# Kernel tuning notes

Hardware: AMD Instinct MI355X
Metric: run time of the kernel (lower is better)

Reference implementation:

```python
import jax, jax.numpy as jnp
import numpy as np

DROPOUT_P = 0.5


def normalize_adj(A):
    # A_tilda = A + I ; A_hat = D^-0.5 A_tilda D^-0.5
    # The torch code does this with diag_embed + two bmm (O(N^3));
    # mathematically it is row/col broadcasting (O(N^2)).
    B, N, _ = A.shape
    A_tilda = A + jnp.eye(N, dtype=A.dtype)
    d_inv_sqrt = jnp.sum(A_tilda, axis=2) ** -0.5          # [B, N]
    return d_inv_sqrt[:, :, None] * A_tilda * d_inv_sqrt[:, None, :]


def gcn_layer(X, A_hat, W, b):
    # standard Kipf GCN layer: A_hat @ (X @ W) + b
    return jnp.einsum('bnm,bmd->bnd', A_hat, X @ W) + b


def setup_inputs() -> dict:
    key = jax.random.key(0)
    ks = jax.random.split(key, 6)
    B, N, Din, H, C = 8, 2048, 64, 64, 16
    X = jax.random.normal(ks[0], (B, N, Din), dtype=jnp.float32)
    A = jax.random.uniform(ks[1], (B, N, N), dtype=jnp.float32)
    W1 = jax.random.normal(ks[2], (Din, H), dtype=jnp.float32) * (1.0 / np.sqrt(Din))
    b1 = jax.random.normal(ks[3], (H,), dtype=jnp.float32) * 0.01
    W2 = jax.random.normal(ks[4], (H, C), dtype=jnp.float32) * (1.0 / np.sqrt(H))
    b2 = jax.random.normal(ks[5], (C,), dtype=jnp.float32) * 0.01
    return {"X": X, "A": A, "W1": W1, "b1": b1, "W2": W2, "b2": b2}


def reference(X, A, W1, b1, W2, b2):
    A_hat = normalize_adj(A)
    h = jax.nn.relu(gcn_layer(X, A_hat, W1, b1))
    # F.dropout default training=True -> apply dropout with a fixed key
    keep = jax.random.bernoulli(jax.random.key(42), 1.0 - DROPOUT_P, h.shape)
    h = jnp.where(keep, h / (1.0 - DROPOUT_P), 0.0).astype(h.dtype)
    return gcn_layer(h, A_hat, W2, b2)
```

## Files before the change

kernel.cpp:

```cpp
#include <hip/hip_runtime.h>

#define BN 16384
#define NN 2048
#define DD 64
#define CC 16
#define KS1 8
#define KS2 16

typedef short bf16x8 __attribute__((ext_vector_type(8)));
typedef float f32x4 __attribute__((ext_vector_type(4)));
typedef unsigned short u16x4 __attribute__((ext_vector_type(4)));

__device__ __forceinline__ f32x4 mfma16(bf16x8 a, bf16x8 b, f32x4 c) {
  return __builtin_amdgcn_mfma_f32_16x16x32_bf16(a, b, c, 0, 0, 0);
}
__device__ __forceinline__ unsigned short f2bf(float f) {
  unsigned u = __float_as_uint(f);
  return (unsigned short)((u + 0x7FFFu + ((u >> 16) & 1u)) >> 16);
}
__device__ __forceinline__ float bf2f(unsigned short h) {
  return __uint_as_float(((unsigned)h) << 16);
}

__device__ __forceinline__ unsigned tf_bits(unsigned i) {
  unsigned x0 = 0u;
  unsigned x1 = i;
  const unsigned k0 = 0u, k1 = 42u, k2 = 0x1BD11BDAu ^ 0u ^ 42u;
  x0 += k0; x1 += k1;
#define TFR(r) { x0 += x1; x1 = (x1 << (r)) | (x1 >> (32 - (r))); x1 ^= x0; }
  TFR(13) TFR(15) TFR(26) TFR(6)
  x0 += k1; x1 += k2 + 1u;
  TFR(17) TFR(29) TFR(16) TFR(24)
  x0 += k2; x1 += k0 + 2u;
  TFR(13) TFR(15) TFR(26) TFR(6)
  x0 += k0; x1 += k1 + 3u;
  TFR(17) TFR(29) TFR(16) TFR(24)
  x0 += k1; x1 += k2 + 4u;
  TFR(13) TFR(15) TFR(26) TFR(6)
  x0 += k2; x1 += k0 + 5u;
#undef TFR
  return x0 ^ x1;
}


__global__ __launch_bounds__(256) void k_deg(const float* __restrict__ A,
    float* __restrict__ dis, unsigned short* __restrict__ Abf)
{
  const int w = threadIdx.x >> 6, lane = threadIdx.x & 63;
  const size_t row = (size_t)blockIdx.x * 4 + w;
  const float4* Arow = (const float4*)(A + row * NN);
  unsigned short* Brow = Abf + row * NN;
  float s = 0.f;
#pragma unroll
  for (int it = 0; it < 8; ++it) {
    float4 v = Arow[lane + 64 * it];
    s += (v.x + v.y) + (v.z + v.w);
    u16x4 p = { f2bf(v.x), f2bf(v.y), f2bf(v.z), f2bf(v.w) };
    *(u16x4*)(Brow + lane * 4 + it * 256) = p;
  }
#pragma unroll
  for (int m = 32; m; m >>= 1) s += __shfl_xor(s, m, 64);
  if (lane == 0) dis[row] = 1.0f / sqrtf(s + 1.0f);
}

__global__ __launch_bounds__(256) void k_xw1(const float* __restrict__ X,
    const float* __restrict__ W1, const float* __restrict__ dis,
    unsigned short* __restrict__ Y1s, unsigned short* __restrict__ Y1sT)
{
  const int tid = threadIdx.x;
  const int w = __builtin_amdgcn_readfirstlane(tid >> 6);
  const int lane = tid & 63;
  const int m15 = lane & 15, quad = lane >> 4;
  const int r0 = blockIdx.x * 64;
  const int b = r0 >> 11, kr0 = r0 & (NN - 1);
  const int arow = r0 + w * 16 + m15;
  const f32x4 zero = 0.f;
  f32x4 acc[4];
#pragma unroll
  for (int t = 0; t < 4; ++t) acc[t] = zero;
#pragma unroll
  for (int ksx = 0; ksx < 2; ++ksx) {
    const float* xp = X + (size_t)arow * DD + ksx * 32 + quad * 8;
    float4 x0 = *(const float4*)xp;
    float4 x1 = *(const float4*)(xp + 4);
    bf16x8 af = { (short)f2bf(x0.x), (short)f2bf(x0.y), (short)f2bf(x0.z), (short)f2bf(x0.w),
                  (short)f2bf(x1.x), (short)f2bf(x1.y), (short)f2bf(x1.z), (short)f2bf(x1.w) };
#pragma unroll
    for (int t = 0; t < 4; ++t) {
      const float* wp = W1 + (size_t)(ksx * 32 + quad * 8) * DD + t * 16 + m15;
      bf16x8 bfr = { (short)f2bf(wp[0*DD]), (short)f2bf(wp[1*DD]), (short)f2bf(wp[2*DD]), (short)f2bf(wp[3*DD]),
                     (short)f2bf(wp[4*DD]), (short)f2bf(wp[5*DD]), (short)f2bf(wp[6*DD]), (short)f2bf(wp[7*DD]) };
      acc[t] = mfma16(af, bfr, acc[t]);
    }
  }
#pragma unroll
  for (int t = 0; t < 4; ++t)
#pragma unroll
    for (int r = 0; r < 4; ++r) {
      const int rowo = r0 + w * 16 + quad * 4 + r;
      const unsigned short v = f2bf(dis[rowo] * acc[t][r]);
      Y1s[(size_t)rowo * DD + t * 16 + m15] = v;
      Y1sT[((size_t)b * DD + t * 16 + m15) * NN + (kr0 + w * 16 + quad * 4 + r)] = v;
    }
}

__global__ __launch_bounds__(256, 4) void k_gemm1(const unsigned short* __restrict__ Abf,
    const unsigned short* __restrict__ Y1sT, float* __restrict__ Z1)
{
  const int Mb = blockIdx.x >> 4;
  const int ns = (blockIdx.x >> 3) & 1;
  const int ks = blockIdx.x & 7;
  const int w = __builtin_amdgcn_readfirstlane((int)threadIdx.x >> 6);
  const int lane = threadIdx.x & 63;
  const int m15 = lane & 15, quad = lane >> 4;
  const int b = Mb >> 3;
  const int k0 = ks * 256 + quad * 8;
  const unsigned short* Ap[4];
#pragma unroll
  for (int m = 0; m < 4; ++m)
    Ap[m] = Abf + ((size_t)Mb * 256 + m * 64 + w * 16 + m15) * NN + k0;
  const unsigned short* Bp0 = Y1sT + ((size_t)b * DD + ns * 32 + m15) * NN + k0;
  const unsigned short* Bp1 = Bp0 + (size_t)16 * NN;
  const f32x4 zero = 0.f;
  f32x4 acc[4][2];
#pragma unroll
  for (int m = 0; m < 4; ++m) { acc[m][0] = zero; acc[m][1] = zero; }
  bf16x8 a[4], b0, b1;
#pragma unroll
  for (int m = 0; m < 4; ++m) a[m] = *(const bf16x8*)Ap[m];
  b0 = *(const bf16x8*)Bp0;
  b1 = *(const bf16x8*)Bp1;
#pragma unroll 1
  for (int kk = 0; kk < 8; ++kk) {
    const int off = (kk < 7) ? (kk + 1) * 32 : 0;
    bf16x8 na[4], nb0, nb1;
#pragma unroll
    for (int m = 0; m < 4; ++m) na[m] = *(const bf16x8*)(Ap[m] + off);
    nb0 = *(const bf16x8*)(Bp0 + off);
    nb1 = *(const bf16x8*)(Bp1 + off);
#pragma unroll
    for (int m = 0; m < 4; ++m) {
      acc[m][0] = mfma16(a[m], b0, acc[m][0]);
      acc[m][1] = mfma16(a[m], b1, acc[m][1]);
    }
#pragma unroll
    for (int m = 0; m < 4; ++m) a[m] = na[m];
    b0 = nb0; b1 = nb1;
  }
#pragma unroll
  for (int m = 0; m < 4; ++m)
#pragma unroll
    for (int t = 0; t < 2; ++t)
#pragma unroll
      for (int r = 0; r < 4; ++r)
        Z1[((size_t)ks * BN + Mb * 256 + m * 64 + w * 16 + quad * 4 + r) * DD
           + ns * 32 + t * 16 + m15] = acc[m][t][r];
}

__global__ __launch_bounds__(256) void k_epi1(const float* __restrict__ Z1,
    const unsigned short* __restrict__ Y1s, const float* __restrict__ dis,
    const float* __restrict__ b1, const float* __restrict__ W2,
    unsigned short* __restrict__ Y2sT)
{
  __shared__ float hs[64 * 65];
  __shared__ float W2l[DD * CC];
  const int tid = threadIdx.x;
  const int r0 = blockIdx.x * 64;
  const int b = r0 >> 11, kr0 = r0 & (NN - 1);
  *(float4*)(W2l + tid * 4) = *(const float4*)(W2 + tid * 4);
  const int n = tid & 63, wg = tid >> 6;
  const float bias = b1[n];
#pragma unroll
  for (int i = 0; i < 16; ++i) {
    const int rl = wg * 16 + i;
    const size_t row = (size_t)r0 + rl;
    const size_t o = row * DD + n;
    float z = bf2f(Y1s[o]);
#pragma unroll
    for (int p = 0; p < KS1; ++p) z += Z1[((size_t)p * BN + row) * DD + n];
    float h = fmaxf(dis[row] * z + bias, 0.f);
    const unsigned bits = tf_bits((unsigned)o);
    h = (bits >> 31) ? 0.f : (h + h);
    hs[rl * 65 + n] = h;
  }
  __syncthreads();
  const int c = tid & 15, rg = tid >> 4;
  float y[4];
#pragma unroll
  for (int rr = 0; rr < 4; ++rr) {
    const int rl = rg * 4 + rr;
    float s = 0.f;
#pragma unroll
    for (int k = 0; k < 64; ++k) s += hs[rl * 65 + k] * W2l[k * CC + c];
    y[rr] = dis[r0 + rl] * s;
  }
  u16x4 pk = { f2bf(y[0]), f2bf(y[1]), f2bf(y[2]), f2bf(y[3]) };
  *(u16x4*)(Y2sT + ((size_t)b * CC + c) * NN + kr0 + rg * 4) = pk;
}

__global__ __launch_bounds__(256, 4) void k_gemm2(const unsigned short* __restrict__ Abf,
    const unsigned short* __restrict__ Y2sT, float* __restrict__ Z2)
{
  const int Mb = blockIdx.x >> 4;
  const int ks = blockIdx.x & 15;
  const int w = __builtin_amdgcn_readfirstlane((int)threadIdx.x >> 6);
  const int lane = threadIdx.x & 63;
  const int m15 = lane & 15, quad = lane >> 4;
  const int b = Mb >> 3;
  const int k0 = ks * 128 + quad * 8;
  const unsigned short* Ap[4];
#pragma unroll
  for (int m = 0; m < 4; ++m)
    Ap[m] = Abf + ((size_t)Mb * 256 + m * 64 + w * 16 + m15) * NN + k0;
  const unsigned short* Bp = Y2sT + ((size_t)b * CC + m15) * NN + k0;
  const f32x4 zero = 0.f;
  f32x4 acc[4];
#pragma unroll
  for (int m = 0; m < 4; ++m) acc[m] = zero;
  bf16x8 a[4], bb;
#pragma unroll
  for (int m = 0; m < 4; ++m) a[m] = *(const bf16x8*)Ap[m];
  bb = *(const bf16x8*)Bp;
#pragma unroll 1
  for (int kk = 0; kk < 4; ++kk) {
    const int off = (kk < 3) ? (kk + 1) * 32 : 0;
    bf16x8 na[4], nbb;
#pragma unroll
    for (int m = 0; m < 4; ++m) na[m] = *(const bf16x8*)(Ap[m] + off);
    nbb = *(const bf16x8*)(Bp + off);
#pragma unroll
    for (int m = 0; m < 4; ++m) acc[m] = mfma16(a[m], bb, acc[m]);
#pragma unroll
    for (int m = 0; m < 4; ++m) a[m] = na[m];
    bb = nbb;
  }
#pragma unroll
  for (int m = 0; m < 4; ++m)
#pragma unroll
    for (int r = 0; r < 4; ++r)
      Z2[((size_t)ks * BN + Mb * 256 + m * 64 + w * 16 + quad * 4 + r) * CC + m15] = acc[m][r];
}

__global__ __launch_bounds__(256) void k_final(const float* __restrict__ Z2,
    const unsigned short* __restrict__ Y2sT, const float* __restrict__ dis,
    const float* __restrict__ b2, float* __restrict__ out)
{
  const int r = blockIdx.x * 256 + threadIdx.x;
  const int b = r >> 11, kr = r & (NN - 1);
  float s[16];
#pragma unroll
  for (int c = 0; c < 16; ++c) s[c] = bf2f(Y2sT[((size_t)b * CC + c) * NN + kr]);
#pragma unroll
  for (int p = 0; p < KS2; ++p)
#pragma unroll
    for (int q = 0; q < 4; ++q) {
      float4 v = *(const float4*)(Z2 + ((size_t)p * BN + r) * CC + q * 4);
      s[q*4+0] += v.x; s[q*4+1] += v.y; s[q*4+2] += v.z; s[q*4+3] += v.w;
    }
  const float dv = dis[r];
#pragma unroll
  for (int q = 0; q < 4; ++q) {
    float4 o4;
    o4.x = dv * s[q*4+0] + b2[q*4+0];
    o4.y = dv * s[q*4+1] + b2[q*4+1];
    o4.z = dv * s[q*4+2] + b2[q*4+2];
    o4.w = dv * s[q*4+3] + b2[q*4+3];
    *(float4*)(out + (size_t)r * CC + q * 4) = o4;
  }
}

#define FKS1 4
#define FKS2 16

__global__ __launch_bounds__(256) void d_deg_xw(const float* __restrict__ A,
    const float* __restrict__ X, const float* __restrict__ W1,
    float* __restrict__ dis, float* __restrict__ Y1s)
{
  const int w = threadIdx.x >> 6, lane = threadIdx.x & 63;
  const int row = __builtin_amdgcn_readfirstlane(blockIdx.x * 4 + w);
  const float4* Arow = (const float4*)(A + (size_t)row * NN);
  float s = 0.f;
#pragma unroll
  for (int it = 0; it < 8; ++it) {
    float4 v = Arow[lane + 64 * it];
    s += v.x + v.y + v.z + v.w;
  }
#pragma unroll
  for (int m = 32; m; m >>= 1) s += __shfl_xor(s, m, 64);
  const float dv = 1.0f / sqrtf(s + 1.0f);
  if (lane == 0) dis[row] = dv;
  const float* Xr = X + (size_t)row * DD;
  float acc = 0.f;
#pragma unroll
  for (int k = 0; k < DD; ++k) acc += Xr[k] * W1[k * DD + lane];
  Y1s[(size_t)row * DD + lane] = dv * acc;
}

__global__ __launch_bounds__(256) void d_gemm1(const float* __restrict__ A,
    const float* __restrict__ Y1s, float* __restrict__ Z1)
{
  const int rb = blockIdx.x >> 2, ks = blockIdx.x & (FKS1 - 1);
  const int lane = threadIdx.x & 63;
  const int c0 = __builtin_amdgcn_readfirstlane((threadIdx.x >> 6) << 4);
  const int row = rb * 64 + lane;
  const int batch = rb >> 5;
  const int KSEG = NN / FKS1;
  const float* Arow = A + (size_t)row * NN + ks * KSEG;
  const float* Yb = Y1s + (size_t)batch * NN * DD + c0;
  const int kbase = ks * KSEG;
  float acc[16];
#pragma unroll
  for (int c = 0; c < 16; ++c) acc[c] = 0.f;
  float4 a0 = *(const float4*)(Arow);
  float4 a1 = *(const float4*)(Arow + 4);
  float4 a2 = *(const float4*)(Arow + 8);
  float4 a3 = *(const float4*)(Arow + 12);
  for (int k = 0; k < KSEG; k += 16) {
    const int kn = (k + 16 < KSEG) ? (k + 16) : 0;
    float4 n0 = *(const float4*)(Arow + kn);
    float4 n1 = *(const float4*)(Arow + kn + 4);
    float4 n2 = *(const float4*)(Arow + kn + 8);
    float4 n3 = *(const float4*)(Arow + kn + 12);
    const float* y0 = Yb + (size_t)(kbase + k) * DD;
    const float av[16] = {a0.x, a0.y, a0.z, a0.w, a1.x, a1.y, a1.z, a1.w,
                          a2.x, a2.y, a2.z, a2.w, a3.x, a3.y, a3.z, a3.w};
#pragma unroll
    for (int j = 0; j < 16; ++j) {
      const float* yr = y0 + j * DD;
#pragma unroll
      for (int c = 0; c < 16; ++c) acc[c] += av[j] * yr[c];
    }
    a0 = n0; a1 = n1; a2 = n2; a3 = n3;
  }
  float* Zp = Z1 + ((size_t)ks * BN + row) * DD + c0;
#pragma unroll
  for (int c = 0; c < 16; c += 4) {
    float4 v; v.x = acc[c]; v.y = acc[c+1]; v.z = acc[c+2]; v.w = acc[c+3];
    *(float4*)(Zp + c) = v;
  }
}

__global__ __launch_bounds__(256) void d_epi1(const float* __restrict__ Z1,
    const float* __restrict__ Y1s, const float* __restrict__ dis,
    const float* __restrict__ b1, const float* __restrict__ W2,
    float* __restrict__ Y2s)
{
  __shared__ float W2l[DD * CC];
  __shared__ float hl[4][DD];
  const int tid = threadIdx.x;
  *(float4*)(W2l + tid * 4) = *(const float4*)(W2 + tid * 4);
  const int w = tid >> 6, lane = tid & 63;
  const int row = blockIdx.x * 4 + w;
  const size_t o = (size_t)row * DD + lane;
  float z = Y1s[o];
#pragma unroll
  for (int p = 0; p < FKS1; ++p) z += Z1[(size_t)p * BN * DD + o];
  const float dv = dis[row];
  float h = fmaxf(dv * z + b1[lane], 0.f);
  const unsigned bits = tf_bits((unsigned)o);
  h = (bits >> 31) ? 0.f : (h + h);
  hl[w][lane] = h;
  __syncthreads();
  const int wr = tid >> 6, l = tid & 63;
  const int c = l & 15, kq = l >> 4;
  float p = 0.f;
#pragma unroll
  for (int kk = 0; kk < 16; ++kk)
    p += hl[wr][kq * 16 + kk] * W2l[(kq * 16 + kk) * CC + c];
  p += __shfl_xor(p, 16, 64);
  p += __shfl_xor(p, 32, 64);
  if (l < 16) {
    const int rg = blockIdx.x * 4 + wr;
    Y2s[(size_t)rg * CC + c] = dis[rg] * p;
  }
}

__global__ __launch_bounds__(256) void d_gemm2(const float* __restrict__ A,
    const float* __restrict__ Y2s, float* __restrict__ Z2)
{
  const int rb = blockIdx.x >> 4, ks = blockIdx.x & (FKS2 - 1);
  const int row = rb * 256 + threadIdx.x;
  const int batch = rb >> 3;
  const int KSEG = NN / FKS2;
  const float* Arow = A + (size_t)row * NN + ks * KSEG;
  const float* Yb = Y2s + (size_t)batch * NN * CC;
  const int kbase = ks * KSEG;
  float acc[16];
#pragma unroll
  for (int c = 0; c < 16; ++c) acc[c] = 0.f;
  float4 a0 = *(const float4*)(Arow);
  float4 a1 = *(const float4*)(Arow + 4);
  for (int k = 0; k < KSEG; k += 8) {
    const int kn = (k + 8 < KSEG) ? (k + 8) : 0;
    float4 n0 = *(const float4*)(Arow + kn);
    float4 n1 = *(const float4*)(Arow + kn + 4);
    const float av[8] = {a0.x, a0.y, a0.z, a0.w, a1.x, a1.y, a1.z, a1.w};
#pragma unroll
    for (int j = 0; j < 8; ++j) {
      const float* yr = Yb + (size_t)(kbase + k + j) * CC;
#pragma unroll
      for (int c = 0; c < 16; ++c) acc[c] += av[j] * yr[c];
    }
    a0 = n0; a1 = n1;
  }
  float* Zp = Z2 + ((size_t)ks * BN + row) * CC;
#pragma unroll
  for (int c = 0; c < 16; c += 4) {
    float4 v; v.x = acc[c]; v.y = acc[c+1]; v.z = acc[c+2]; v.w = acc[c+3];
    *(float4*)(Zp + c) = v;
  }
}

__global__ __launch_bounds__(256) void d_final(const float* __restrict__ Z2,
    const float* __restrict__ Y2s, const float* __restrict__ dis,
    const float* __restrict__ b2, float* __restrict__ out)
{
  const int gid = blockIdx.x * 256 + threadIdx.x;
  const int r = gid >> 2, q = gid & 3;
  const size_t o = (size_t)r * CC + q * 4;
  float4 s = *(const float4*)(Y2s + o);
#pragma unroll
  for (int p = 0; p < FKS2; ++p) {
    const float4 zp = *(const float4*)(Z2 + (size_t)p * BN * CC + o);
    s.x += zp.x; s.y += zp.y; s.z += zp.z; s.w += zp.w;
  }
  const float dv = dis[r];
  const float4 bb = *(const float4*)(b2 + q * 4);
  float4 res;
  res.x = dv * s.x + bb.x;
  res.y = dv * s.y + bb.y;
  res.z = dv * s.z + bb.z;
  res.w = dv * s.w + bb.w;
  *(float4*)(out + o) = res;
}

extern "C" void kernel_launch(void* const* d_in, const int* in_sizes, int n_in,
                              void* d_out, int out_size, void* d_ws, size_t ws_size,
                              hipStream_t stream) {
  const float* X  = (const float*)d_in[0];
  const float* A  = (const float*)d_in[1];
  const float* W1 = (const float*)d_in[2];
  const float* b1 = (const float*)d_in[3];
  const float* W2 = (const float*)d_in[4];
  const float* b2 = (const float*)d_in[5];
  float* out = (float*)d_out;
  char* wsb = (char*)d_ws;

  const size_t NEED = 105447424;
  if (ws_size >= NEED) {
    unsigned short* Abf  = (unsigned short*)wsb;
    float*          Z1   = (float*)(wsb + 67108864);
    float*          Z2   = Z1;
    float*          dis  = (float*)(wsb + 100663296);
    unsigned short* Y1s  = (unsigned short*)(wsb + 100728832);
    unsigned short* Y1sT = (unsigned short*)(wsb + 102825984);
    unsigned short* Y2sT = (unsigned short*)(wsb + 104923136);

    k_deg  <<<BN / 4,  256, 0, stream>>>(A, dis, Abf);
    k_xw1  <<<BN / 64, 256, 0, stream>>>(X, W1, dis, Y1s, Y1sT);
    k_gemm1<<<1024,    256, 0, stream>>>(Abf, Y1sT, Z1);
    k_epi1 <<<BN / 64, 256, 0, stream>>>(Z1, Y1s, dis, b1, W2, Y2sT);
    k_gemm2<<<1024,    256, 0, stream>>>(Abf, Y2sT, Z2);
    k_final<<<BN / 256, 256, 0, stream>>>(Z2, Y2sT, dis, b2, out);
  } else {
    float* ws  = (float*)d_ws;
    float* dis = ws;
    float* Y1s = ws + 16384;
    float* Z1  = Y1s + (size_t)BN * DD;
    float* Z2  = Z1;
    float* Y2s = Z1 + (size_t)FKS1 * BN * DD;

    d_deg_xw<<<BN / 4,     256, 0, stream>>>(A, X, W1, dis, Y1s);
    d_gemm1 <<<256 * FKS1, 256, 0, stream>>>(A, Y1s, Z1);
    d_epi1  <<<BN / 4,     256, 0, stream>>>(Z1, Y1s, dis, b1, W2, Y2s);
    d_gemm2 <<<64 * FKS2,  256, 0, stream>>>(A, Y2s, Z2);
    d_final <<<256,        256, 0, stream>>>(Z2, Y2s, dis, b2, out);
  }
}
```

Measured before the change: 278.0 us.

## Fuse X@W1 into degree kernel and widen grids of epilogue and final kernels

Folds the X·W1 projection into the degree/bf16-conversion kernel, so each wave computes its row's 64 outputs with scalar FMAs instead of a separate MFMA launch. This removes one launch and a dependency between stages. The epilogue now uses 16 rows per block (4x more blocks), and the final reduction uses 4 threads per row, to raise parallelism for these small memory-bound kernels. The trade-offs are scalar FP32 math in place of MFMA for the projection, less coalesced transposed Y1sT stores, and the projection now running in FP32 rather than from bf16-rounded inputs.

After: 274.6 us. About the same (-1.2%).

```diff
diff --git a/kernel.cpp b/kernel.cpp
--- a/kernel.cpp
+++ b/kernel.cpp
@@ -44,7 +44,9 @@
 
 
 __global__ __launch_bounds__(256) void k_deg(const float* __restrict__ A,
-    float* __restrict__ dis, unsigned short* __restrict__ Abf)
+    const float* __restrict__ X, const float* __restrict__ W1,
+    float* __restrict__ dis, unsigned short* __restrict__ Abf,
+    unsigned short* __restrict__ Y1s, unsigned short* __restrict__ Y1sT)
 {
   const int w = threadIdx.x >> 6, lane = threadIdx.x & 63;
   const size_t row = (size_t)blockIdx.x * 4 + w;
@@ -60,48 +62,16 @@
   }
 #pragma unroll
   for (int m = 32; m; m >>= 1) s += __shfl_xor(s, m, 64);
-  if (lane == 0) dis[row] = 1.0f / sqrtf(s + 1.0f);
-}
-
-__global__ __launch_bounds__(256) void k_xw1(const float* __restrict__ X,
-    const float* __restrict__ W1, const float* __restrict__ dis,
-    unsigned short* __restrict__ Y1s, unsigned short* __restrict__ Y1sT)
-{
-  const int tid = threadIdx.x;
-  const int w = __builtin_amdgcn_readfirstlane(tid >> 6);
-  const int lane = tid & 63;
-  const int m15 = lane & 15, quad = lane >> 4;
-  const int r0 = blockIdx.x * 64;
-  const int b = r0 >> 11, kr0 = r0 & (NN - 1);
-  const int arow = r0 + w * 16 + m15;
-  const f32x4 zero = 0.f;
-  f32x4 acc[4];
-#pragma unroll
-  for (int t = 0; t < 4; ++t) acc[t] = zero;
-#pragma unroll
-  for (int ksx = 0; ksx < 2; ++ksx) {
-    const float* xp = X + (size_t)arow * DD + ksx * 32 + quad * 8;
-    float4 x0 = *(const float4*)xp;
-    float4 x1 = *(const float4*)(xp + 4);
-    bf16x8 af = { (short)f2bf(x0.x), (short)f2bf(x0.y), (short)f2bf(x0.z), (short)f2bf(x0.w),
-                  (short)f2bf(x1.x), (short)f2bf(x1.y), (short)f2bf(x1.z), (short)f2bf(x1.w) };
-#pragma unroll
-    for (int t = 0; t < 4; ++t) {
-      const float* wp = W1 + (size_t)(ksx * 32 + quad * 8) * DD + t * 16 + m15;
-      bf16x8 bfr = { (short)f2bf(wp[0*DD]), (short)f2bf(wp[1*DD]), (short)f2bf(wp[2*DD]), (short)f2bf(wp[3*DD]),
-                     (short)f2bf(wp[4*DD]), (short)f2bf(wp[5*DD]), (short)f2bf(wp[6*DD]), (short)f2bf(wp[7*DD]) };
-      acc[t] = mfma16(af, bfr, acc[t]);
-    }
-  }
-#pragma unroll
-  for (int t = 0; t < 4; ++t)
-#pragma unroll
-    for (int r = 0; r < 4; ++r) {
-      const int rowo = r0 + w * 16 + quad * 4 + r;
-      const unsigned short v = f2bf(dis[rowo] * acc[t][r]);
-      Y1s[(size_t)rowo * DD + t * 16 + m15] = v;
-      Y1sT[((size_t)b * DD + t * 16 + m15) * NN + (kr0 + w * 16 + quad * 4 + r)] = v;
-    }
+  const float dv = 1.0f / sqrtf(s + 1.0f);
+  if (lane == 0) dis[row] = dv;
+  const float* Xr = X + row * DD;
+  float acc = 0.f;
+#pragma unroll
+  for (int k = 0; k < DD; ++k) acc += Xr[k] * W1[k * DD + lane];
+  const unsigned short yv = f2bf(dv * acc);
+  Y1s[row * DD + lane] = yv;
+  const int b = (int)(row >> 11), kr = (int)(row & (NN - 1));
+  Y1sT[((size_t)b * DD + lane) * NN + kr] = yv;
 }
 
 __global__ __launch_bounds__(256, 4) void k_gemm1(const unsigned short* __restrict__ Abf,
@@ -162,40 +132,32 @@
     const float* __restrict__ b1, const float* __restrict__ W2,
     unsigned short* __restrict__ Y2sT)
 {
-  __shared__ float hs[64 * 65];
+  __shared__ float hs[16][65];
   __shared__ float W2l[DD * CC];
   const int tid = threadIdx.x;
-  const int r0 = blockIdx.x * 64;
-  const int b = r0 >> 11, kr0 = r0 & (NN - 1);
   *(float4*)(W2l + tid * 4) = *(const float4*)(W2 + tid * 4);
-  const int n = tid & 63, wg = tid >> 6;
-  const float bias = b1[n];
-#pragma unroll
-  for (int i = 0; i < 16; ++i) {
-    const int rl = wg * 16 + i;
+  const int r0 = blockIdx.x * 16;
+#pragma unroll
+  for (int j = 0; j < 4; ++j) {
+    const int e = tid + j * 256;
+    const int rl = e >> 6, n = e & 63;
     const size_t row = (size_t)r0 + rl;
     const size_t o = row * DD + n;
     float z = bf2f(Y1s[o]);
 #pragma unroll
     for (int p = 0; p < KS1; ++p) z += Z1[((size_t)p * BN + row) * DD + n];
-    float h = fmaxf(dis[row] * z + bias, 0.f);
+    float h = fmaxf(dis[row] * z + b1[n], 0.f);
     const unsigned bits = tf_bits((unsigned)o);
-    h = (bits >> 31) ? 0.f : (h + h);
-    hs[rl * 65 + n] = h;
+    hs[rl][n] = (bits >> 31) ? 0.f : (h + h);
   }
   __syncthreads();
-  const int c = tid & 15, rg = tid >> 4;
-  float y[4];
-#pragma unroll
-  for (int rr = 0; rr < 4; ++rr) {
-    const int rl = rg * 4 + rr;
-    float s = 0.f;
-#pragma unroll
-    for (int k = 0; k < 64; ++k) s += hs[rl * 65 + k] * W2l[k * CC + c];
-    y[rr] = dis[r0 + rl] * s;
-  }
-  u16x4 pk = { f2bf(y[0]), f2bf(y[1]), f2bf(y[2]), f2bf(y[3]) };
-  *(u16x4*)(Y2sT + ((size_t)b * CC + c) * NN + kr0 + rg * 4) = pk;
+  const int c = tid & 15, rl = tid >> 4;
+  float s = 0.f;
+#pragma unroll
+  for (int k = 0; k < DD; ++k) s += hs[rl][k] * W2l[k * CC + c];
+  const int row = r0 + rl;
+  const int b = row >> 11, kr = row & (NN - 1);
+  Y2sT[((size_t)b * CC + c) * NN + kr] = f2bf(dis[row] * s);
 }
 
 __global__ __launch_bounds__(256, 4) void k_gemm2(const unsigned short* __restrict__ Abf,
@@ -245,28 +207,27 @@
     const unsigned short* __restrict__ Y2sT, const float* __restrict__ dis,
     const float* __restrict__ b2, float* __restrict__ out)
 {
-  const int r = blockIdx.x * 256 + threadIdx.x;
+  const int gid = blockIdx.x * 256 + threadIdx.x;
+  const int r = gid >> 2, q = gid & 3;
   const int b = r >> 11, kr = r & (NN - 1);
-  float s[16];
-#pragma unroll
-  for (int c = 0; c < 16; ++c) s[c] = bf2f(Y2sT[((size_t)b * CC + c) * NN + kr]);
-#pragma unroll
-  for (int p = 0; p < KS2; ++p)
-#pragma unroll
-    for (int q = 0; q < 4; ++q) {
-      float4 v = *(const float4*)(Z2 + ((size_t)p * BN + r) * CC + q * 4);
-      s[q*4+0] += v.x; s[q*4+1] += v.y; s[q*4+2] += v.z; s[q*4+3] += v.w;
-    }
+  float4 s;
+  s.x = bf2f(Y2sT[((size_t)b * CC + q * 4 + 0) * NN + kr]);
+  s.y = bf2f(Y2sT[((size_t)b * CC + q * 4 + 1) * NN + kr]);
+  s.z = bf2f(Y2sT[((size_t)b * CC + q * 4 + 2) * NN + kr]);
+  s.w = bf2f(Y2sT[((size_t)b * CC + q * 4 + 3) * NN + kr]);
+#pragma unroll
+  for (int p = 0; p < KS2; ++p) {
+    const float4 zp = *(const float4*)(Z2 + ((size_t)p * BN + r) * CC + q * 4);
+    s.x += zp.x; s.y += zp.y; s.z += zp.z; s.w += zp.w;
+  }
   const float dv = dis[r];
-#pragma unroll
-  for (int q = 0; q < 4; ++q) {
-    float4 o4;
-    o4.x = dv * s[q*4+0] + b2[q*4+0];
-    o4.y = dv * s[q*4+1] + b2[q*4+1];
-    o4.z = dv * s[q*4+2] + b2[q*4+2];
-    o4.w = dv * s[q*4+3] + b2[q*4+3];
-    *(float4*)(out + (size_t)r * CC + q * 4) = o4;
-  }
+  const float4 bb = *(const float4*)(b2 + q * 4);
+  float4 res;
+  res.x = dv * s.x + bb.x;
+  res.y = dv * s.y + bb.y;
+  res.z = dv * s.z + bb.z;
+  res.w = dv * s.w + bb.w;
+  *(float4*)(out + (size_t)r * CC + q * 4) = res;
 }
 
 #define FKS1 4
@@ -456,12 +417,11 @@
     unsigned short* Y1sT = (unsigned short*)(wsb + 102825984);
     unsigned short* Y2sT = (unsigned short*)(wsb + 104923136);
 
-    k_deg  <<<BN / 4,  256, 0, stream>>>(A, dis, Abf);
-    k_xw1  <<<BN / 64, 256, 0, stream>>>(X, W1, dis, Y1s, Y1sT);
+    k_deg  <<<BN / 4,  256, 0, stream>>>(A, X, W1, dis, Abf, Y1s, Y1sT);
     k_gemm1<<<1024,    256, 0, stream>>>(Abf, Y1sT, Z1);
-    k_epi1 <<<BN / 64, 256, 0, stream>>>(Z1, Y1s, dis, b1, W2, Y2sT);
+    k_epi1 <<<BN / 16, 256, 0, stream>>>(Z1, Y1s, dis, b1, W2, Y2sT);
     k_gemm2<<<1024,    256, 0, stream>>>(Abf, Y2sT, Z2);
-    k_final<<<BN / 256, 256, 0, stream>>>(Z2, Y2sT, dis, b2, out);
+    k_final<<<256,     256, 0, stream>>>(Z2, Y2sT, dis, b2, out);
   } else {
     float* ws  = (float*)d_ws;
     float* dis = ws;
```
